# Performance work log

Hardware: AMD Instinct MI355X
Metric: run time of the kernel (lower is better)

The kernel has to match this reference:

```python
import jax, jax.numpy as jnp
import numpy as np

B, T, I, H = 64, 512, 256, 256


def setup_inputs() -> dict:
    key = jax.random.key(0)
    ks = jax.random.split(key, 5)
    s = 1.0 / np.sqrt(H)
    return {
        "x": jax.random.normal(ks[0], (B, T, I), dtype=jnp.float32),
        "W_ih": jax.random.uniform(ks[1], (4 * H, I), jnp.float32, -s, s),
        "W_hh": jax.random.uniform(ks[2], (4 * H, H), jnp.float32, -s, s),
        "b_ih": jax.random.uniform(ks[3], (4 * H,), jnp.float32, -s, s),
        "b_hh": jax.random.uniform(ks[4], (4 * H,), jnp.float32, -s, s),
    }


def reference(x, W_ih, W_hh, b_ih, b_hh):
    # PyTorch LSTM gate order: input, forget, cell(g), output.
    # Precompute input projection for all timesteps: [B, T, 4H]
    x_proj = jnp.einsum("bti,gi->btg", x, W_ih) + b_ih + b_hh

    def step(carry, xt):
        h, c = carry                       # [B, H] each
        gates = xt + h @ W_hh.T            # [B, 4H]
        i, f, g, o = jnp.split(gates, 4, axis=-1)
        i = jax.nn.sigmoid(i)
        f = jax.nn.sigmoid(f)
        g = jnp.tanh(g)
        o = jax.nn.sigmoid(o)
        c = f * c + i * g
        h = o * jnp.tanh(c)
        return (h, c), h

    h0 = jnp.zeros((x.shape[0], W_hh.shape[1]), x.dtype)
    c0 = jnp.zeros_like(h0)
    (hT, cT), ys = jax.lax.scan(step, (h0, c0), jnp.swapaxes(x_proj, 0, 1))
    y = jnp.swapaxes(ys, 0, 1)             # [B, T, H], batch_first
    # Matches torch: (output, (h_n, c_n)) with num_layers*num_dirs = 1
    return y, hT[None], cT[None]
```

## Files before the change

### kernel.cpp

```cpp
#include <hip/hip_runtime.h>
#include <hip/hip_bf16.h>
#include <stdint.h>

#define Bz 64
#define Tz 512
#define Iz 256
#define Hz 256
#define G4z 1024
#define YSZ (Bz*Tz*Hz)

typedef __bf16 bf16;
typedef float  f32x4  __attribute__((ext_vector_type(4)));
typedef int    i32x4  __attribute__((ext_vector_type(4)));
typedef __bf16 bf16x8 __attribute__((ext_vector_type(8)));
typedef __bf16 bf16x4 __attribute__((ext_vector_type(4)));

#define XP_OFF  0u
#define XB_OFF  67108864u
#define WI_OFF  83886080u

__global__ __launch_bounds__(256) void cvt_f32_bf16(const float* __restrict__ in,
                                                    bf16* __restrict__ out, int n4) {
  int i = blockIdx.x * blockDim.x + threadIdx.x;
  if (i >= n4) return;
  float4 v = reinterpret_cast<const float4*>(in)[i];
  bf16x4 o = {(__bf16)v.x, (__bf16)v.y, (__bf16)v.z, (__bf16)v.w};
  *reinterpret_cast<bf16x4*>(out + (size_t)i*4) = o;
}

__global__ __launch_bounds__(256) void xproj_gemm(const bf16* __restrict__ A,
                                                  const bf16* __restrict__ Bw,
                                                  const float* __restrict__ b_ih,
                                                  const float* __restrict__ b_hh,
                                                  bf16* __restrict__ xp) {
  constexpr int K = 256;
  __shared__ __align__(16) bf16 As[128*32];
  __shared__ __align__(16) bf16 Bs[128*32];
  __shared__ float bias_s[128];
  const int bm = blockIdx.x >> 3;
  const int bn = blockIdx.x & 7;
  const int m0 = bm * 128, n0 = bn * 128;
  const int tid = threadIdx.x;
  if (tid < 128) bias_s[tid] = b_ih[n0 + tid] + b_hh[n0 + tid];
  const int w = tid >> 6, lane = tid & 63;
  const int wm = w >> 1, wn = w & 1;
  const int lr = lane & 15, lk = lane >> 4;
  f32x4 acc[4][4] = {};
  for (int kt = 0; kt < 8; ++kt) {
#pragma unroll
    for (int p = 0; p < 2; ++p) {
      int elem = p * 256 + tid;
      int row = elem >> 2, c = elem & 3;
      uint4 va = *reinterpret_cast<const uint4*>(A + (size_t)(m0 + row) * K + kt*32 + c*8);
      *reinterpret_cast<uint4*>((char*)As + row*64 + ((c ^ (row & 3)) * 16)) = va;
      uint4 vb = *reinterpret_cast<const uint4*>(Bw + (size_t)(n0 + row) * K + kt*32 + c*8);
      *reinterpret_cast<uint4*>((char*)Bs + row*64 + ((c ^ (row & 3)) * 16)) = vb;
    }
    __syncthreads();
    bf16x8 fa[4], fb[4];
#pragma unroll
    for (int f = 0; f < 4; ++f) {
      int ra = wm*64 + f*16 + lr;
      fa[f] = *reinterpret_cast<const bf16x8*>((char*)As + ra*64 + ((lk ^ (ra & 3)) * 16));
      int rb = wn*64 + f*16 + lr;
      fb[f] = *reinterpret_cast<const bf16x8*>((char*)Bs + rb*64 + ((lk ^ (rb & 3)) * 16));
    }
#pragma unroll
    for (int fi = 0; fi < 4; ++fi)
#pragma unroll
      for (int fj = 0; fj < 4; ++fj)
        acc[fi][fj] = __builtin_amdgcn_mfma_f32_16x16x32_bf16(fa[fi], fb[fj], acc[fi][fj], 0, 0, 0);
    __syncthreads();
  }
#pragma unroll
  for (int fi = 0; fi < 4; ++fi)
#pragma unroll
    for (int fj = 0; fj < 4; ++fj) {
      int col = n0 + wn*64 + fj*16 + lr;
      float bias = bias_s[wn*64 + fj*16 + lr];
#pragma unroll
      for (int v = 0; v < 4; ++v) {
        int row = m0 + wm*64 + fi*16 + lk*4 + v;
        xp[(size_t)row * 1024 + col] = (__bf16)(acc[fi][fj][v] + bias);
      }
    }
}


__device__ __forceinline__ int sdot4f(int a, int b, int c) {
#if __has_builtin(__builtin_amdgcn_sdot4)
  return __builtin_amdgcn_sdot4(a, b, c, false);
#else
  int r = c;
  r += (int)(signed char)(a)        * (int)(signed char)(b);
  r += (int)(signed char)(a >> 8)   * (int)(signed char)(b >> 8);
  r += (int)(signed char)(a >> 16)  * (int)(signed char)(b >> 16);
  r += (int)(signed char)(a >> 24)  * (int)(signed char)(b >> 24);
  return r;
#endif
}
__device__ __forceinline__ float pair_xor1(float v) {
#if __has_builtin(__builtin_amdgcn_mov_dpp)
  return __int_as_float(__builtin_amdgcn_mov_dpp(__float_as_int(v), 0xB1, 0xf, 0xf, true));
#else
  return __shfl_xor(v, 1);
#endif
}
#define SCL (1.0f / (2032.0f * 127.0f))

__global__ __launch_bounds__(512, 2) void lstm_rec(const bf16* __restrict__ xp,
                                                   const float* __restrict__ Whh,
                                                   float* __restrict__ out) {
  __shared__ __align__(16) char h_s[2][256];
  const int tid = threadIdx.x;
  const int b = blockIdx.x;
  const int h = tid >> 1;
  const int s = tid & 1;
  const int r0 = s * 256 + h;
  const int r1 = r0 + 512;

  int w0[64], w1[64];
  {
    const float* wp0 = Whh + (size_t)r0 * 256;
    const float* wp1 = Whh + (size_t)r1 * 256;
#pragma unroll
    for (int d = 0; d < 64; ++d) {
      float4 f = *reinterpret_cast<const float4*>(wp0 + d*4);
      int q0 = (int)rintf(f.x * 2032.f), q1 = (int)rintf(f.y * 2032.f);
      int q2 = (int)rintf(f.z * 2032.f), q3 = (int)rintf(f.w * 2032.f);
      w0[d] = (q0 & 255) | ((q1 & 255) << 8) | ((q2 & 255) << 16) | ((q3 & 255) << 24);
      float4 g = *reinterpret_cast<const float4*>(wp1 + d*4);
      int p0 = (int)rintf(g.x * 2032.f), p1 = (int)rintf(g.y * 2032.f);
      int p2 = (int)rintf(g.z * 2032.f), p3 = (int)rintf(g.w * 2032.f);
      w1[d] = (p0 & 255) | ((p1 & 255) << 8) | ((p2 & 255) << 16) | ((p3 & 255) << 24);
    }
  }
  if (tid < 64) reinterpret_cast<int*>(h_s[0])[tid] = 0;

  const bf16* xprow = xp + (size_t)b * Tz * 1024;
  unsigned short c0 = *(const unsigned short*)(xprow + r0);
  unsigned short c1 = *(const unsigned short*)(xprow + r1);
  unsigned short n0 = *(const unsigned short*)(xprow + 1024 + r0);
  unsigned short n1 = *(const unsigned short*)(xprow + 1024 + r1);

  float cc = 0.f;
  __syncthreads();

  for (int t = 0; t < Tz; ++t) {
    const char* hb = h_s[t & 1];
    unsigned short f0 = 0, f1 = 0;
    if (t + 2 < Tz) {
      f0 = *(const unsigned short*)(xprow + (size_t)(t+2)*1024 + r0);
      f1 = *(const unsigned short*)(xprow + (size_t)(t+2)*1024 + r1);
    }
    int a0=0,a1=0,a2=0,a3=0, d0=0,d1=0,d2=0,d3=0;
#pragma unroll
    for (int d = 0; d < 16; ++d) {
      i32x4 hv = *reinterpret_cast<const i32x4*>(hb + d*16);
      a0 = sdot4f(hv[0], w0[4*d+0], a0);
      a1 = sdot4f(hv[1], w0[4*d+1], a1);
      a2 = sdot4f(hv[2], w0[4*d+2], a2);
      a3 = sdot4f(hv[3], w0[4*d+3], a3);
      d0 = sdot4f(hv[0], w1[4*d+0], d0);
      d1 = sdot4f(hv[1], w1[4*d+1], d1);
      d2 = sdot4f(hv[2], w1[4*d+2], d2);
      d3 = sdot4f(hv[3], w1[4*d+3], d3);
    }
    float g0 = (float)((a0 + a1) + (a2 + a3)) * SCL + __uint_as_float((unsigned)c0 << 16);
    float g1 = (float)((d0 + d1) + (d2 + d3)) * SCL + __uint_as_float((unsigned)c1 << 16);
    float e0 = __expf(-g0);
    float act0 = __builtin_amdgcn_rcpf(1.f + e0);
    float in1 = s ? -g1 : 2.f * g1;
    float e1 = __expf(in1);
    float dr = __builtin_amdgcn_rcpf(1.f + e1);
    float act1 = s ? dr : 1.f - 2.f * dr;
    float x0 = pair_xor1(act0);
    float x1 = pair_xor1(act1);
    float gi = s ? x0 : act0;
    float gf = s ? act0 : x0;
    float gg = s ? x1 : act1;
    float go = s ? act1 : x1;
    cc = gf * cc + gi * gg;
    float e2 = __expf(2.f * cc);
    float hv = go * (1.f - 2.f * __builtin_amdgcn_rcpf(1.f + e2));
    if (!s) {
      out[((size_t)b * Tz + t) * 256 + h] = hv;
      if (t < Tz - 1) {
        h_s[(t & 1) ^ 1][h] = (char)(int)rintf(hv * 127.f);
      } else {
        out[(size_t)YSZ + (size_t)b * 256 + h] = hv;
        out[(size_t)YSZ + 16384 + (size_t)b * 256 + h] = cc;
      }
    }
    if (t == Tz - 1) break;
    c0 = n0; c1 = n1; n0 = f0; n1 = f1;
    asm volatile("s_waitcnt lgkmcnt(0)\n\ts_barrier" ::: "memory");
  }
}

extern "C" void kernel_launch(void* const* d_in, const int* in_sizes, int n_in,
                              void* d_out, int out_size, void* d_ws, size_t ws_size,
                              hipStream_t stream) {
  const float* x    = (const float*)d_in[0];
  const float* W_ih = (const float*)d_in[1];
  const float* W_hh = (const float*)d_in[2];
  const float* b_ih = (const float*)d_in[3];
  const float* b_hh = (const float*)d_in[4];
  float* out = (float*)d_out;
  char* ws = (char*)d_ws;

  bf16* xp  = (bf16*)(ws + XP_OFF);
  bf16* xb  = (bf16*)(ws + XB_OFF);
  bf16* wib = (bf16*)(ws + WI_OFF);

  cvt_f32_bf16<<<8192, 256, 0, stream>>>(x, xb, (Bz*Tz*Iz) / 4);
  cvt_f32_bf16<<<256, 256, 0, stream>>>(W_ih, wib, (G4z*Iz) / 4);
  xproj_gemm<<<2048, 256, 0, stream>>>(xb, wib, b_ih, b_hh, xp);
  lstm_rec<<<64, 512, 0, stream>>>(xp, W_hh, out);
}
```

Measured before the change: 598.4 us.

## Split recurrent dot products along K across thread pairs instead of gate rows

Each thread pair now splits the hidden dimension in half. Each thread computes partial dot products for all four gates of one hidden unit over 128 inputs, then combines them with a DPP pair-exchange of integer partial sums. Previously each thread computed two full-length gate rows and exchanged activations. Each thread now reads only half of the h vector from LDS per step, which roughly halves LDS traffic per thread, and both threads compute every activation redundantly. The cost is four cross-lane exchanges in place of two, and redundant transcendental work on both threads.

Result: slower. 661.5 us (+10.5%).

```diff
diff --git a/kernel.cpp b/kernel.cpp
--- a/kernel.cpp
+++ b/kernel.cpp
@@ -15,9 +15,29 @@
 typedef __bf16 bf16x8 __attribute__((ext_vector_type(8)));
 typedef __bf16 bf16x4 __attribute__((ext_vector_type(4)));
 
-#define XP_OFF  0u
-#define XB_OFF  67108864u
-#define WI_OFF  83886080u
+#define XP_OFF   0u
+#define XB_OFF   67108864u
+#define WI_OFF   83886080u
+
+__device__ __forceinline__ int sdot4f(int a, int b, int c) {
+#if __has_builtin(__builtin_amdgcn_sdot4)
+  return __builtin_amdgcn_sdot4(a, b, c, false);
+#else
+  int r = c;
+  r += (int)(signed char)(a)        * (int)(signed char)(b);
+  r += (int)(signed char)(a >> 8)   * (int)(signed char)(b >> 8);
+  r += (int)(signed char)(a >> 16)  * (int)(signed char)(b >> 16);
+  r += (int)(signed char)(a >> 24)  * (int)(signed char)(b >> 24);
+  return r;
+#endif
+}
+__device__ __forceinline__ int pair_xor1_i(int v) {
+#if __has_builtin(__builtin_amdgcn_mov_dpp)
+  return __builtin_amdgcn_mov_dpp(v, 0xB1, 0xf, 0xf, true);
+#else
+  return __shfl_xor(v, 1);
+#endif
+}
 
 __global__ __launch_bounds__(256) void cvt_f32_bf16(const float* __restrict__ in,
                                                     bf16* __restrict__ out, int n4) {
@@ -87,25 +107,6 @@
 }
 
 
-__device__ __forceinline__ int sdot4f(int a, int b, int c) {
-#if __has_builtin(__builtin_amdgcn_sdot4)
-  return __builtin_amdgcn_sdot4(a, b, c, false);
-#else
-  int r = c;
-  r += (int)(signed char)(a)        * (int)(signed char)(b);
-  r += (int)(signed char)(a >> 8)   * (int)(signed char)(b >> 8);
-  r += (int)(signed char)(a >> 16)  * (int)(signed char)(b >> 16);
-  r += (int)(signed char)(a >> 24)  * (int)(signed char)(b >> 24);
-  return r;
-#endif
-}
-__device__ __forceinline__ float pair_xor1(float v) {
-#if __has_builtin(__builtin_amdgcn_mov_dpp)
-  return __int_as_float(__builtin_amdgcn_mov_dpp(__float_as_int(v), 0xB1, 0xf, 0xf, true));
-#else
-  return __shfl_xor(v, 1);
-#endif
-}
 #define SCL (1.0f / (2032.0f * 127.0f))
 
 __global__ __launch_bounds__(512, 2) void lstm_rec(const bf16* __restrict__ xp,
@@ -115,75 +116,68 @@
   const int tid = threadIdx.x;
   const int b = blockIdx.x;
   const int h = tid >> 1;
-  const int s = tid & 1;
-  const int r0 = s * 256 + h;
-  const int r1 = r0 + 512;
-
-  int w0[64], w1[64];
-  {
-    const float* wp0 = Whh + (size_t)r0 * 256;
-    const float* wp1 = Whh + (size_t)r1 * 256;
-#pragma unroll
-    for (int d = 0; d < 64; ++d) {
-      float4 f = *reinterpret_cast<const float4*>(wp0 + d*4);
+  const int half = tid & 1;
+  const int kf = half * 128;
+
+  int w[4][32];
+#pragma unroll
+  for (int q = 0; q < 4; ++q) {
+    const float* wp = Whh + (size_t)(q*256 + h) * 256 + kf;
+#pragma unroll
+    for (int d = 0; d < 32; ++d) {
+      float4 f = *reinterpret_cast<const float4*>(wp + d*4);
       int q0 = (int)rintf(f.x * 2032.f), q1 = (int)rintf(f.y * 2032.f);
       int q2 = (int)rintf(f.z * 2032.f), q3 = (int)rintf(f.w * 2032.f);
-      w0[d] = (q0 & 255) | ((q1 & 255) << 8) | ((q2 & 255) << 16) | ((q3 & 255) << 24);
-      float4 g = *reinterpret_cast<const float4*>(wp1 + d*4);
-      int p0 = (int)rintf(g.x * 2032.f), p1 = (int)rintf(g.y * 2032.f);
-      int p2 = (int)rintf(g.z * 2032.f), p3 = (int)rintf(g.w * 2032.f);
-      w1[d] = (p0 & 255) | ((p1 & 255) << 8) | ((p2 & 255) << 16) | ((p3 & 255) << 24);
+      w[q][d] = (q0 & 255) | ((q1 & 255) << 8) | ((q2 & 255) << 16) | ((q3 & 255) << 24);
     }
   }
   if (tid < 64) reinterpret_cast<int*>(h_s[0])[tid] = 0;
 
   const bf16* xprow = xp + (size_t)b * Tz * 1024;
-  unsigned short c0 = *(const unsigned short*)(xprow + r0);
-  unsigned short c1 = *(const unsigned short*)(xprow + r1);
-  unsigned short n0 = *(const unsigned short*)(xprow + 1024 + r0);
-  unsigned short n1 = *(const unsigned short*)(xprow + 1024 + r1);
+  unsigned short cur[4], nxt[4];
+#pragma unroll
+  for (int q = 0; q < 4; ++q) {
+    cur[q] = *(const unsigned short*)(xprow + q*256 + h);
+    nxt[q] = *(const unsigned short*)(xprow + 1024 + q*256 + h);
+  }
 
   float cc = 0.f;
   __syncthreads();
 
   for (int t = 0; t < Tz; ++t) {
-    const char* hb = h_s[t & 1];
-    unsigned short f0 = 0, f1 = 0;
+    const char* hb = h_s[t & 1] + kf;
+    unsigned short fut[4] = {0, 0, 0, 0};
     if (t + 2 < Tz) {
-      f0 = *(const unsigned short*)(xprow + (size_t)(t+2)*1024 + r0);
-      f1 = *(const unsigned short*)(xprow + (size_t)(t+2)*1024 + r1);
-    }
-    int a0=0,a1=0,a2=0,a3=0, d0=0,d1=0,d2=0,d3=0;
-#pragma unroll
-    for (int d = 0; d < 16; ++d) {
+#pragma unroll
+      for (int q = 0; q < 4; ++q)
+        fut[q] = *(const unsigned short*)(xprow + (size_t)(t+2)*1024 + q*256 + h);
+    }
+    int A0[4] = {}, A1[4] = {}, A2[4] = {}, A3[4] = {};
+#pragma unroll
+    for (int d = 0; d < 8; ++d) {
       i32x4 hv = *reinterpret_cast<const i32x4*>(hb + d*16);
-      a0 = sdot4f(hv[0], w0[4*d+0], a0);
-      a1 = sdot4f(hv[1], w0[4*d+1], a1);
-      a2 = sdot4f(hv[2], w0[4*d+2], a2);
-      a3 = sdot4f(hv[3], w0[4*d+3], a3);
-      d0 = sdot4f(hv[0], w1[4*d+0], d0);
-      d1 = sdot4f(hv[1], w1[4*d+1], d1);
-      d2 = sdot4f(hv[2], w1[4*d+2], d2);
-      d3 = sdot4f(hv[3], w1[4*d+3], d3);
-    }
-    float g0 = (float)((a0 + a1) + (a2 + a3)) * SCL + __uint_as_float((unsigned)c0 << 16);
-    float g1 = (float)((d0 + d1) + (d2 + d3)) * SCL + __uint_as_float((unsigned)c1 << 16);
-    float e0 = __expf(-g0);
-    float act0 = __builtin_amdgcn_rcpf(1.f + e0);
-    float in1 = s ? -g1 : 2.f * g1;
-    float e1 = __expf(in1);
-    float dr = __builtin_amdgcn_rcpf(1.f + e1);
-    float act1 = s ? dr : 1.f - 2.f * dr;
-    float x0 = pair_xor1(act0);
-    float x1 = pair_xor1(act1);
-    float gi = s ? x0 : act0;
-    float gf = s ? act0 : x0;
-    float gg = s ? x1 : act1;
-    float go = s ? act1 : x1;
+#pragma unroll
+      for (int q = 0; q < 4; ++q) {
+        A0[q] = sdot4f(hv[0], w[q][d*4+0], A0[q]);
+        A1[q] = sdot4f(hv[1], w[q][d*4+1], A1[q]);
+        A2[q] = sdot4f(hv[2], w[q][d*4+2], A2[q]);
+        A3[q] = sdot4f(hv[3], w[q][d*4+3], A3[q]);
+      }
+    }
+    float g[4];
+#pragma unroll
+    for (int q = 0; q < 4; ++q) {
+      int s4 = (A0[q] + A1[q]) + (A2[q] + A3[q]);
+      int tot = s4 + pair_xor1_i(s4);
+      g[q] = (float)tot * SCL + __uint_as_float((unsigned)cur[q] << 16);
+    }
+    float gi = __builtin_amdgcn_rcpf(1.f + __expf(-g[0]));
+    float gf = __builtin_amdgcn_rcpf(1.f + __expf(-g[1]));
+    float gg = 1.f - 2.f * __builtin_amdgcn_rcpf(__expf(2.f * g[2]) + 1.f);
+    float go = __builtin_amdgcn_rcpf(1.f + __expf(-g[3]));
     cc = gf * cc + gi * gg;
-    float e2 = __expf(2.f * cc);
-    float hv = go * (1.f - 2.f * __builtin_amdgcn_rcpf(1.f + e2));
-    if (!s) {
+    float hv = go * (1.f - 2.f * __builtin_amdgcn_rcpf(__expf(2.f * cc) + 1.f));
+    if (!half) {
       out[((size_t)b * Tz + t) * 256 + h] = hv;
       if (t < Tz - 1) {
         h_s[(t & 1) ^ 1][h] = (char)(int)rintf(hv * 127.f);
@@ -193,7 +187,8 @@
       }
     }
     if (t == Tz - 1) break;
-    c0 = n0; c1 = n1; n0 = f0; n1 = f1;
+#pragma unroll
+    for (int q = 0; q < 4; ++q) { cur[q] = nxt[q]; nxt[q] = fut[q]; }
     asm volatile("s_waitcnt lgkmcnt(0)\n\ts_barrier" ::: "memory");
   }
 }
```
